# Kernel tuning notes

Measured on AMD Instinct MI355X. Metric: run time of the kernel, lower is better.

## Reference

```python
import jax, jax.numpy as jnp
import numpy as np

NB_NODE = 100000
FT = 256
OUT_FT = 256
NB_REL = 4
BATCH = 8192
DEG = 16  # padded neighbors per (node, relation)


def setup_inputs() -> dict:
    key = jax.random.key(0)
    k1, k2, k3, k4 = jax.random.split(key, 4)
    features = jax.random.normal(k1, (NB_NODE, FT), dtype=jnp.float32)
    neighbor_idx = jax.random.randint(k2, (BATCH, NB_REL, DEG), 0, NB_NODE, dtype=jnp.int32)
    # per-relation GCN weight, scaled like xavier
    W = jax.random.normal(k3, (NB_REL, FT, OUT_FT), dtype=jnp.float32) * (1.0 / np.sqrt(FT))
    b = jnp.zeros((NB_REL, OUT_FT), dtype=jnp.float32)
    prelu_a = jnp.full((1,), 0.25, dtype=jnp.float32)  # nn.PReLU() default single param
    node_list = jax.random.randint(k4, (BATCH,), 0, NB_NODE, dtype=jnp.int32)
    return {"features": features, "neighbor_idx": neighbor_idx, "W": W, "b": b,
            "prelu_a": prelu_a, "node_list": node_list, "k": 0}


def _prelu(x, a):
    return jnp.where(x >= 0, x, a * x)


def reference(features, neighbor_idx, W, b, prelu_a, node_list, k):
    # Ragged per-relation neighbor gather + mean (vectorized form of the
    # python double loop): [B, R, D, F] -> mean over D -> [B, R, F]
    v_in = jnp.mean(features[neighbor_idx], axis=2)
    # Per-relation GCN linear + PReLU: [B, R, F] x [R, F, O] -> [B, R, O]
    h = jnp.einsum('brf,rfo->bro', v_in, W) + b[None, :, :]
    h = _prelu(h, prelu_a[0])
    # isAtt=False branch: mean over relations -> [B, O]
    return jnp.mean(h, axis=1)
```

## Files before the change

kernel.cpp:

```cpp
#include <hip/hip_runtime.h>

#define B_TOT 8192
#define FT    256
#define NREL  4
#define DEG   16
#define BM    16

typedef __attribute__((ext_vector_type(8))) short bf16x8;
typedef __attribute__((ext_vector_type(4))) float f32x4;

static __device__ __forceinline__ unsigned short f2bf(float x) {
    union { float f; unsigned int u; } c; c.f = x;
    unsigned int u = c.u;
    u += 0x7fffu + ((u >> 16) & 1u);
    return (unsigned short)(u >> 16);
}
static __device__ __forceinline__ float bf2f(unsigned short h) {
    union { unsigned int u; float f; } c; c.u = ((unsigned int)h) << 16;
    return c.f;
}

__global__ __launch_bounds__(256) void cvt_feat_k(const float* __restrict__ f,
                                                  unsigned short* __restrict__ fb,
                                                  int n4) {
    int i = blockIdx.x * 256 + threadIdx.x;
    if (i < n4) {
        float4 x = ((const float4*)f)[i];
        ushort4 o;
        o.x = f2bf(x.x); o.y = f2bf(x.y); o.z = f2bf(x.z); o.w = f2bf(x.w);
        ((ushort4*)fb)[i] = o;
    }
}

__global__ __launch_bounds__(256) void wtrans_k(const float* __restrict__ W,
                                                unsigned short* __restrict__ Wt) {
    __shared__ float t[64][65];
    int r = blockIdx.z, ft = blockIdx.y, ot = blockIdx.x;
    int c = threadIdx.x & 63, rw = threadIdx.x >> 6;
    const float* src = W + ((size_t)r * 256 + ft * 64) * 256 + ot * 64;
#pragma unroll
    for (int i = 0; i < 16; ++i) {
        int row = i * 4 + rw;
        t[row][c] = src[(size_t)row * 256 + c];
    }
    __syncthreads();
    unsigned short* dst = Wt + ((size_t)r * 256 + ot * 64) * 256 + ft * 64;
#pragma unroll
    for (int i = 0; i < 16; ++i) {
        int row = i * 4 + rw;
        dst[(size_t)row * 256 + c] = f2bf(t[c][row]);
    }
}

template <bool BF16TAB>
__global__ __launch_bounds__(1024, 8) void fused_k(const void* __restrict__ ftab_,
                                                   const int* __restrict__ nidx,
                                                   const unsigned short* __restrict__ Wt,
                                                   const float* __restrict__ bias,
                                                   const float* __restrict__ prelu,
                                                   float* __restrict__ out) {
    __shared__ int shIdx[BM * NREL * DEG];
    __shared__ unsigned short As[NREL][BM][FT + 8];
    const int tid  = threadIdx.x;
    const int lane = tid & 63, w = tid >> 6;
    const int blk  = blockIdx.x;
    const int mrow = lane & 15, quad = lane >> 4;
    const float pa = prelu[0];

    shIdx[tid] = nidx[(size_t)blk * (BM * NREL * DEG) + tid];
    __syncthreads();

    const float inv = 1.0f / 16.0f;
    if constexpr (BF16TAB) {
        const unsigned short* fb = (const unsigned short*)ftab_;
#pragma unroll
        for (int rr = 0; rr < NREL; ++rr) {
            const int* ip = shIdx + (w * NREL + rr) * DEG;
            ushort4 x[DEG];
#pragma unroll
            for (int t = 0; t < DEG; ++t)
                x[t] = ((const ushort4*)(fb + (size_t)ip[t] * FT))[lane];
            float s0 = 0.f, s1 = 0.f, s2 = 0.f, s3 = 0.f;
#pragma unroll
            for (int t = 0; t < DEG; ++t) {
                s0 += bf2f(x[t].x); s1 += bf2f(x[t].y);
                s2 += bf2f(x[t].z); s3 += bf2f(x[t].w);
            }
            ushort4 o;
            o.x = f2bf(s0 * inv); o.y = f2bf(s1 * inv);
            o.z = f2bf(s2 * inv); o.w = f2bf(s3 * inv);
            *(ushort4*)(&As[rr][w][lane * 4]) = o;
        }
    } else {
        const float* ff = (const float*)ftab_;
#pragma unroll
        for (int rr = 0; rr < NREL; ++rr) {
            const int* ip = shIdx + (w * NREL + rr) * DEG;
            float s0 = 0.f, s1 = 0.f, s2 = 0.f, s3 = 0.f;
#pragma unroll
            for (int h = 0; h < 2; ++h) {
                float4 x[8];
#pragma unroll
                for (int t = 0; t < 8; ++t)
                    x[t] = ((const float4*)(ff + (size_t)ip[h * 8 + t] * FT))[lane];
#pragma unroll
                for (int t = 0; t < 8; ++t) {
                    s0 += x[t].x; s1 += x[t].y; s2 += x[t].z; s3 += x[t].w;
                }
            }
            ushort4 o;
            o.x = f2bf(s0 * inv); o.y = f2bf(s1 * inv);
            o.z = f2bf(s2 * inv); o.w = f2bf(s3 * inv);
            *(ushort4*)(&As[rr][w][lane * 4]) = o;
        }
    }
    __syncthreads();

    const int ncol = w * 16 + mrow;
    f32x4 accO = {};
#pragma unroll
    for (int r = 0; r < NREL; ++r) {
        const unsigned short* bp = Wt + ((size_t)(r * 256 + ncol)) * FT;
        const float bv = bias[r * 256 + ncol];
        f32x4 acc = {};
#pragma unroll
        for (int kk = 0; kk < 8; ++kk) {
            const int k0 = kk * 32 + quad * 8;
            const bf16x8 a = *(const bf16x8*)(&As[r][mrow][k0]);
            const bf16x8 b = *(const bf16x8*)(bp + k0);
            acc = __builtin_amdgcn_mfma_f32_16x16x32_bf16(a, b, acc, 0, 0, 0);
        }
#pragma unroll
        for (int i = 0; i < 4; ++i) {
            float h = acc[i] + bv;
            h = (h >= 0.f) ? h : pa * h;
            accO[i] += h;
        }
    }

    const size_t rbase = (size_t)(blk * BM + quad * 4) * 256 + ncol;
#pragma unroll
    for (int i = 0; i < 4; ++i)
        out[rbase + (size_t)i * 256] = accO[i] * 0.25f;
}

extern "C" void kernel_launch(void* const* d_in, const int* in_sizes, int n_in,
                              void* d_out, int out_size, void* d_ws, size_t ws_size,
                              hipStream_t stream) {
    const float* feat  = (const float*)d_in[0];
    const int*   nidx  = (const int*)  d_in[1];
    const float* W     = (const float*)d_in[2];
    const float* bias  = (const float*)d_in[3];
    const float* prelu = (const float*)d_in[4];
    float* out = (float*)d_out;

    const size_t feat_elems = (size_t)in_sizes[0];
    const size_t fb_bytes = feat_elems * 2;
    const size_t wt_bytes = (size_t)NREL * 256 * FT * 2;

    if (ws_size >= fb_bytes + wt_bytes) {
        unsigned short* fb = (unsigned short*)d_ws;
        unsigned short* Wt = fb + feat_elems;
        int n4 = (int)(feat_elems / 4);
        cvt_feat_k<<<(n4 + 255) / 256, 256, 0, stream>>>(feat, fb, n4);
        wtrans_k<<<dim3(4, 4, 4), 256, 0, stream>>>(W, Wt);
        fused_k<true><<<B_TOT / BM, 1024, 0, stream>>>(fb, nidx, Wt, bias, prelu, out);
    } else {
        unsigned short* Wt = (unsigned short*)d_ws;
        wtrans_k<<<dim3(4, 4, 4), 256, 0, stream>>>(W, Wt);
        fused_k<false><<<B_TOT / BM, 1024, 0, stream>>>(feat, nidx, Wt, bias, prelu, out);
    }
}
```

Before: 229.9 us.

## Gather neighbor rows via direct global-to-LDS loads with double-buffered pipeline

The bf16 path now uses 512-thread blocks where each wave gathers neighbor rows through global_load_lds into a double-buffered LDS staging area, overlapping the next chunk's loads with accumulation of the current one. Each wave also computes two 16-column MFMA tiles instead of one, halving the wave count per block. This aims to cut register pressure and hide gather latency, but it adds LDS usage and relies on manual vmcnt waits. Gather concurrency per wave drops compared with the previous 16 outstanding loads.

After: 230.2 us. Within noise of the previous version (+0.1%).

```diff
diff --git a/kernel.cpp b/kernel.cpp
--- a/kernel.cpp
+++ b/kernel.cpp
@@ -52,13 +52,108 @@
     }
 }
 
-template <bool BF16TAB>
-__global__ __launch_bounds__(1024, 8) void fused_k(const void* __restrict__ ftab_,
-                                                   const int* __restrict__ nidx,
-                                                   const unsigned short* __restrict__ Wt,
-                                                   const float* __restrict__ bias,
-                                                   const float* __restrict__ prelu,
-                                                   float* __restrict__ out) {
+__global__ __launch_bounds__(512, 4) void fused_dma_k(const unsigned short* __restrict__ fb,
+                                                      const int* __restrict__ nidx,
+                                                      const unsigned short* __restrict__ Wt,
+                                                      const float* __restrict__ bias,
+                                                      const float* __restrict__ prelu,
+                                                      float* __restrict__ out) {
+    __shared__ int shIdx[BM * NREL * DEG];
+    __shared__ unsigned short raw[8][2][1024];
+    __shared__ unsigned short As[NREL][BM][FT + 8];
+    const int tid  = threadIdx.x;
+    const int lane = tid & 63, w = tid >> 6;
+    const int l32  = lane & 31, half = lane >> 5;
+    const int mrow = lane & 15, quad = lane >> 4;
+    const int blk  = blockIdx.x;
+    const float pa = prelu[0];
+
+    ((int2*)shIdx)[tid] = ((const int2*)(nidx + (size_t)blk * (BM * NREL * DEG)))[tid];
+    __syncthreads();
+
+    const int mbase = w * 2;
+    auto issue = [&](int c) {
+        const int g = c >> 2, sub = c & 3;
+        const int m = mbase + (g & 1), rel = g >> 1;
+        const int* ib = shIdx + (m * NREL + rel) * DEG + sub * 4;
+        unsigned short* slot = &raw[w][c & 1][0];
+        const unsigned short* gA = fb + (size_t)ib[half]     * FT + l32 * 8;
+        const unsigned short* gB = fb + (size_t)ib[2 + half] * FT + l32 * 8;
+        __builtin_amdgcn_global_load_lds(
+            (const __attribute__((address_space(1))) void*)gA,
+            (__attribute__((address_space(3))) void*)&slot[lane * 8], 16, 0, 0);
+        __builtin_amdgcn_global_load_lds(
+            (const __attribute__((address_space(1))) void*)gB,
+            (__attribute__((address_space(3))) void*)&slot[512 + lane * 8], 16, 0, 0);
+    };
+
+    float s0 = 0.f, s1 = 0.f, s2 = 0.f, s3 = 0.f;
+    const float inv = 1.0f / 16.0f;
+    issue(0);
+#pragma unroll
+    for (int c = 0; c < 32; ++c) {
+        if (c + 1 < 32) issue(c + 1);
+        if (c + 1 < 32) asm volatile("s_waitcnt vmcnt(2)" ::: "memory");
+        else            asm volatile("s_waitcnt vmcnt(0)" ::: "memory");
+        if ((c & 3) == 0) { s0 = s1 = s2 = s3 = 0.f; }
+        const unsigned short* slot = &raw[w][c & 1][0];
+#pragma unroll
+        for (int j = 0; j < 4; ++j) {
+            const ushort4 x = *(const ushort4*)(slot + j * 256 + lane * 4);
+            s0 += bf2f(x.x); s1 += bf2f(x.y); s2 += bf2f(x.z); s3 += bf2f(x.w);
+        }
+        if ((c & 3) == 3) {
+            const int g = c >> 2;
+            const int m = mbase + (g & 1), rel = g >> 1;
+            ushort4 o;
+            o.x = f2bf(s0 * inv); o.y = f2bf(s1 * inv);
+            o.z = f2bf(s2 * inv); o.w = f2bf(s3 * inv);
+            *(ushort4*)(&As[rel][m][lane * 4]) = o;
+        }
+    }
+    __syncthreads();
+
+    const int ncol0 = w * 32 + mrow;
+    f32x4 accO[2] = {};
+#pragma unroll
+    for (int r = 0; r < NREL; ++r) {
+        const unsigned short* bp0 = Wt + ((size_t)(r * 256 + ncol0)) * FT;
+        const unsigned short* bp1 = bp0 + 16 * FT;
+        const float bv0 = bias[r * 256 + ncol0];
+        const float bv1 = bias[r * 256 + ncol0 + 16];
+        f32x4 acc[2] = {};
+#pragma unroll
+        for (int kk = 0; kk < 8; ++kk) {
+            const int k0 = kk * 32 + quad * 8;
+            const bf16x8 a  = *(const bf16x8*)(&As[r][mrow][k0]);
+            const bf16x8 b0 = *(const bf16x8*)(bp0 + k0);
+            const bf16x8 b1 = *(const bf16x8*)(bp1 + k0);
+            acc[0] = __builtin_amdgcn_mfma_f32_16x16x32_bf16(a, b0, acc[0], 0, 0, 0);
+            acc[1] = __builtin_amdgcn_mfma_f32_16x16x32_bf16(a, b1, acc[1], 0, 0, 0);
+        }
+#pragma unroll
+        for (int i = 0; i < 4; ++i) {
+            float h0 = acc[0][i] + bv0; h0 = (h0 >= 0.f) ? h0 : pa * h0;
+            float h1 = acc[1][i] + bv1; h1 = (h1 >= 0.f) ? h1 : pa * h1;
+            accO[0][i] += h0;
+            accO[1][i] += h1;
+        }
+    }
+
+    const size_t rbase = (size_t)(blk * BM + quad * 4) * 256 + ncol0;
+#pragma unroll
+    for (int i = 0; i < 4; ++i) {
+        out[rbase + (size_t)i * 256]      = accO[0][i] * 0.25f;
+        out[rbase + (size_t)i * 256 + 16] = accO[1][i] * 0.25f;
+    }
+}
+
+__global__ __launch_bounds__(1024, 8) void fused_reg_k(const float* __restrict__ ff,
+                                                       const int* __restrict__ nidx,
+                                                       const unsigned short* __restrict__ Wt,
+                                                       const float* __restrict__ bias,
+                                                       const float* __restrict__ prelu,
+                                                       float* __restrict__ out) {
     __shared__ int shIdx[BM * NREL * DEG];
     __shared__ unsigned short As[NREL][BM][FT + 8];
     const int tid  = threadIdx.x;
@@ -71,48 +166,25 @@
     __syncthreads();
 
     const float inv = 1.0f / 16.0f;
-    if constexpr (BF16TAB) {
-        const unsigned short* fb = (const unsigned short*)ftab_;
-#pragma unroll
-        for (int rr = 0; rr < NREL; ++rr) {
-            const int* ip = shIdx + (w * NREL + rr) * DEG;
-            ushort4 x[DEG];
-#pragma unroll
-            for (int t = 0; t < DEG; ++t)
-                x[t] = ((const ushort4*)(fb + (size_t)ip[t] * FT))[lane];
-            float s0 = 0.f, s1 = 0.f, s2 = 0.f, s3 = 0.f;
-#pragma unroll
-            for (int t = 0; t < DEG; ++t) {
-                s0 += bf2f(x[t].x); s1 += bf2f(x[t].y);
-                s2 += bf2f(x[t].z); s3 += bf2f(x[t].w);
+#pragma unroll
+    for (int rr = 0; rr < NREL; ++rr) {
+        const int* ip = shIdx + (w * NREL + rr) * DEG;
+        float s0 = 0.f, s1 = 0.f, s2 = 0.f, s3 = 0.f;
+#pragma unroll
+        for (int h = 0; h < 2; ++h) {
+            float4 x[8];
+#pragma unroll
+            for (int t = 0; t < 8; ++t)
+                x[t] = ((const float4*)(ff + (size_t)ip[h * 8 + t] * FT))[lane];
+#pragma unroll
+            for (int t = 0; t < 8; ++t) {
+                s0 += x[t].x; s1 += x[t].y; s2 += x[t].z; s3 += x[t].w;
             }
-            ushort4 o;
-            o.x = f2bf(s0 * inv); o.y = f2bf(s1 * inv);
-            o.z = f2bf(s2 * inv); o.w = f2bf(s3 * inv);
-            *(ushort4*)(&As[rr][w][lane * 4]) = o;
-        }
-    } else {
-        const float* ff = (const float*)ftab_;
-#pragma unroll
-        for (int rr = 0; rr < NREL; ++rr) {
-            const int* ip = shIdx + (w * NREL + rr) * DEG;
-            float s0 = 0.f, s1 = 0.f, s2 = 0.f, s3 = 0.f;
-#pragma unroll
-            for (int h = 0; h < 2; ++h) {
-                float4 x[8];
-#pragma unroll
-                for (int t = 0; t < 8; ++t)
-                    x[t] = ((const float4*)(ff + (size_t)ip[h * 8 + t] * FT))[lane];
-#pragma unroll
-                for (int t = 0; t < 8; ++t) {
-                    s0 += x[t].x; s1 += x[t].y; s2 += x[t].z; s3 += x[t].w;
-                }
-            }
-            ushort4 o;
-            o.x = f2bf(s0 * inv); o.y = f2bf(s1 * inv);
-            o.z = f2bf(s2 * inv); o.w = f2bf(s3 * inv);
-            *(ushort4*)(&As[rr][w][lane * 4]) = o;
-        }
+        }
+        ushort4 o;
+        o.x = f2bf(s0 * inv); o.y = f2bf(s1 * inv);
+        o.z = f2bf(s2 * inv); o.w = f2bf(s3 * inv);
+        *(ushort4*)(&As[rr][w][lane * 4]) = o;
     }
     __syncthreads();
 
@@ -137,7 +209,6 @@
             accO[i] += h;
         }
     }
-
     const size_t rbase = (size_t)(blk * BM + quad * 4) * 256 + ncol;
 #pragma unroll
     for (int i = 0; i < 4; ++i)
@@ -164,10 +235,10 @@
         int n4 = (int)(feat_elems / 4);
         cvt_feat_k<<<(n4 + 255) / 256, 256, 0, stream>>>(feat, fb, n4);
         wtrans_k<<<dim3(4, 4, 4), 256, 0, stream>>>(W, Wt);
-        fused_k<true><<<B_TOT / BM, 1024, 0, stream>>>(fb, nidx, Wt, bias, prelu, out);
+        fused_dma_k<<<B_TOT / BM, 512, 0, stream>>>(fb, nidx, Wt, bias, prelu, out);
     } else {
         unsigned short* Wt = (unsigned short*)d_ws;
         wtrans_k<<<dim3(4, 4, 4), 256, 0, stream>>>(W, Wt);
-        fused_k<false><<<B_TOT / BM, 1024, 0, stream>>>(feat, nidx, Wt, bias, prelu, out);
-    }
-}
+        fused_reg_k<<<B_TOT / BM, 1024, 0, stream>>>(feat, nidx, Wt, bias, prelu, out);
+    }
+}
```
